# Kernel optimization log

Measured on AMD Instinct MI355X. Metric: run time of the kernel, lower is better.

Reference implementation:

```python
import jax, jax.numpy as jnp
import numpy as np

DIM = 256
NUM_HEADS = 4
HEAD_DIM = DIM // NUM_HEADS
SCALE = HEAD_DIM ** -0.5
LOGIT_CLAMP = 6.0


def _conv1x1(x, w, b):
    # x: (B,C,H,W), w: (Cout,Cin), b: (Cout,)
    return jnp.einsum('bchw,oc->bohw', x, w) + b[None, :, None, None]


def setup_inputs() -> dict:
    key = jax.random.key(0)
    ks = jax.random.split(key, 10)
    B, C, H, W = 8, DIM, 48, 48
    init = lambda k, shape, fan_in: jax.random.normal(k, shape, jnp.float32) * (fan_in ** -0.5)
    return {
        'src_feat': jax.random.normal(ks[0], (B, C, H, W), jnp.float32),
        'tgt_feat': jax.random.normal(ks[1], (B, C, H, W), jnp.float32),
        'qw': init(ks[2], (DIM, DIM), DIM), 'qb': jnp.zeros((DIM,), jnp.float32),
        'kw': init(ks[3], (DIM, DIM), DIM), 'kb': jnp.zeros((DIM,), jnp.float32),
        'vw': init(ks[4], (DIM, DIM), DIM), 'vb': jnp.zeros((DIM,), jnp.float32),
        'ow': init(ks[5], (DIM, DIM), DIM), 'ob': jnp.zeros((DIM,), jnp.float32),
    }


def reference(src_feat, tgt_feat, qw, qb, kw, kb, vw, vb, ow, ob):
    B, C, H, W = src_feat.shape
    N = H * W
    Q = _conv1x1(src_feat, qw, qb)
    K = _conv1x1(tgt_feat, kw, kb)
    V = _conv1x1(tgt_feat, vw, vb)
    # (B,C,H,W) -> (B,heads,head_dim,N) -> (B,heads,N,head_dim)
    to_heads = lambda t: t.reshape(B, NUM_HEADS, HEAD_DIM, N).transpose(0, 1, 3, 2)
    Qh, Kh, Vh = to_heads(Q), to_heads(K), to_heads(V)
    attn = jnp.einsum('bhnd,bhmd->bhnm', Qh, Kh) * SCALE
    attn = jnp.clip(attn, -LOGIT_CLAMP, LOGIT_CLAMP)
    attn = jax.nn.softmax(attn, axis=-1)
    out = jnp.einsum('bhnm,bhmd->bhnd', attn, Vh)
    out = out.transpose(0, 1, 3, 2).reshape(B, C, H, W)
    return _conv1x1(out, ow, ob)
```

## Files before the change

kernel.cpp:

```cpp
#include <hip/hip_runtime.h>
#include <hip/hip_bf16.h>

#define DIM 256
#define NHEADS 4
#define HDIM 64
#define NPIX 2304
#define NBATCH 8
#define KCN 72
#define NTN 144
#define SCALE_L2E 0.18033688011112042f
#define CLAMP_L2E 8.656170245332781f

typedef __hip_bfloat16 bf16;
typedef __bf16 bf16x8 __attribute__((ext_vector_type(8)));
typedef float  f32x4  __attribute__((ext_vector_type(4)));
typedef float  f32x16 __attribute__((ext_vector_type(16)));

__device__ __forceinline__ unsigned int pack2bf(float a, float b) {
    __hip_bfloat162 h = __float22bfloat162_rn(float2{a, b});
    union { __hip_bfloat162 h; unsigned int u; } c; c.h = h;
    return c.u;
}

__global__ __launch_bounds__(256) void cvt_w_kernel(
    const float* __restrict__ w0, const float* __restrict__ w1,
    const float* __restrict__ w2, const float* __restrict__ w3,
    bf16* __restrict__ out)
{
    const int sel = blockIdx.y;
    const float* src = sel == 0 ? w0 : sel == 1 ? w1 : sel == 2 ? w2 : w3;
    const int i = blockIdx.x * 256 + threadIdx.x;
    const int m = i >> 5, c0 = (i & 31) * 8;
    const int mh = m >> 7, mt = (m >> 4) & 7, lo = m & 15;
    const int kc = c0 >> 5, hi = (c0 >> 3) & 3;
    float4 a = *(const float4*)(src + i * 8);
    float4 b = *(const float4*)(src + i * 8 + 4);
    uint4 u;
    u.x = pack2bf(a.x, a.y); u.y = pack2bf(a.z, a.w);
    u.z = pack2bf(b.x, b.y); u.w = pack2bf(b.z, b.w);
    const size_t fb = (((size_t)(mh * 8 + kc)) * 8 + mt) * 512 + (hi * 16 + lo) * 8;
    *(uint4*)(void*)(out + (size_t)sel * 65536 + fb) = u;
}

__global__ __launch_bounds__(256) void txp_kernel(
    const float* __restrict__ src, const float* __restrict__ tgt,
    bf16* __restrict__ oS, bf16* __restrict__ oT)
{
    const int b = blockIdx.z & 7;
    const float* in = (blockIdx.z >> 3) ? tgt : src;
    bf16* out = (blockIdx.z >> 3) ? oT : oS;
    const int n0 = blockIdx.x * 64, c0 = blockIdx.y * 64;
    __shared__ float tile[64][65];
    const int t = threadIdx.x;
#pragma unroll
    for (int i = 0; i < 4; ++i) {
        int idx = t + i * 256;
        int cl = idx >> 4, n4 = (idx & 15) * 4;
        float4 v = *(const float4*)(in + ((size_t)b * DIM + c0 + cl) * NPIX + n0 + n4);
        tile[cl][n4] = v.x; tile[cl][n4 + 1] = v.y;
        tile[cl][n4 + 2] = v.z; tile[cl][n4 + 3] = v.w;
    }
    __syncthreads();
#pragma unroll
    for (int i = 0; i < 2; ++i) {
        int idx = t + i * 256;
        int nl = idx >> 3, c8 = (idx & 7) * 8;
        uint4 u;
        u.x = pack2bf(tile[c8 + 0][nl], tile[c8 + 1][nl]);
        u.y = pack2bf(tile[c8 + 2][nl], tile[c8 + 3][nl]);
        u.z = pack2bf(tile[c8 + 4][nl], tile[c8 + 5][nl]);
        u.w = pack2bf(tile[c8 + 6][nl], tile[c8 + 7][nl]);
        const int n = n0 + nl, c = c0 + c8;
        const size_t fb = (((size_t)(b * NTN + (n >> 4))) * 8 + (c >> 5)) * 512
                        + ((((c >> 3) & 3) * 16) + (n & 15)) * 8;
        *(uint4*)(void*)(out + fb) = u;
    }
}

__device__ __forceinline__ void conv_core(
    const bf16* __restrict__ xp, const bf16* __restrict__ wp,
    int wk, f32x4 (&acc)[8])
{
#pragma unroll
    for (int mt = 0; mt < 8; ++mt) acc[mt] = (f32x4){0.f, 0.f, 0.f, 0.f};

    const int kbase = wk * 4;
    bf16x8 a = *(const bf16x8*)(const void*)(xp + (size_t)kbase * 512);
    bf16x8 bfr[8];
#pragma unroll
    for (int mt = 0; mt < 8; ++mt)
        bfr[mt] = *(const bf16x8*)(const void*)(wp + (size_t)(kbase * 8 + mt) * 512);

#pragma unroll
    for (int ki = 0; ki < 4; ++ki) {
        const int kn = kbase + ((ki + 1) & 3);
        bf16x8 a2 = *(const bf16x8*)(const void*)(xp + (size_t)kn * 512);
        bf16x8 bfr2[8];
#pragma unroll
        for (int mt = 0; mt < 8; ++mt)
            bfr2[mt] = *(const bf16x8*)(const void*)(wp + (size_t)(kn * 8 + mt) * 512);
#pragma unroll
        for (int mt = 0; mt < 8; ++mt)
            acc[mt] = __builtin_amdgcn_mfma_f32_16x16x32_bf16(a, bfr[mt], acc[mt], 0, 0, 0);
        a = a2;
#pragma unroll
        for (int mt = 0; mt < 8; ++mt) bfr[mt] = bfr2[mt];
    }
}

__global__ __launch_bounds__(256, 3) void conv_qkv_kernel(
    const bf16* __restrict__ XS, const bf16* __restrict__ XT,
    const bf16* __restrict__ Wbf,
    const float* __restrict__ qb, const float* __restrict__ kb2,
    const float* __restrict__ vb2,
    bf16* __restrict__ Qt, bf16* __restrict__ Kt, bf16* __restrict__ Vt)
{
    const int b  = blockIdx.z;
    const int sel = blockIdx.y >> 1, mh = blockIdx.y & 1;
    const int n0 = blockIdx.x * 32;
    const int w  = threadIdx.x >> 6, l = threadIdx.x & 63;
    const int wn = w & 1, wk = w >> 1;
    const int lo = l & 15, hi = l >> 4;

    __shared__ float red[2][64][36];

    const bf16* X = sel == 0 ? XS : XT;
    const float* bias = sel == 0 ? qb : sel == 1 ? kb2 : vb2;
    const float scale = sel == 0 ? SCALE_L2E : 1.0f;
    bf16* Yb = sel == 0 ? Qt : sel == 1 ? Kt : Vt;

    const int ntile = blockIdx.x * 2 + wn;
    const bf16* xp = X + ((size_t)(b * NTN + ntile) * 8) * 512 + l * 8;
    const bf16* wp = Wbf + (size_t)sel * 65536 + (size_t)mh * 32768 + l * 8;

    f32x4 acc[8];
    conv_core(xp, wp, wk, acc);

    if (wk == 1) {
#pragma unroll
        for (int mt = 0; mt < 8; ++mt)
            *(float4*)&red[wn][l][mt * 4] = make_float4(acc[mt][0], acc[mt][1],
                                                        acc[mt][2], acc[mt][3]);
    }
    __syncthreads();
    if (wk != 0) return;

#pragma unroll
    for (int mt = 0; mt < 8; ++mt) {
        float4 v = *(float4*)&red[wn][l][mt * 4];
        acc[mt][0] += v.x; acc[mt][1] += v.y; acc[mt][2] += v.z; acc[mt][3] += v.w;
    }

    const int nb = n0 + wn * 16 + hi * 4;
#pragma unroll
    for (int mt = 0; mt < 8; ++mt) {
        const int m = mh * 128 + mt * 16 + lo;
        const float bv = bias[m];
        if (sel < 2) {
            const int h = m >> 6, d = m & 63;
            const size_t fb = (((size_t)(b * NHEADS + h) * KCN + (nb >> 5)) * 4 + (d >> 4)) * 512
                            + ((((d >> 3) & 1) * 32) + (nb & 31)) * 8 + (d & 7);
#pragma unroll
            for (int r = 0; r < 4; ++r)
                Yb[fb + r * 8] = __float2bfloat16((acc[mt][r] + bv) * scale);
        } else {
            const int h = m >> 6, dv = m & 63;
            const size_t fb = ((((size_t)(b * NHEADS + h) * KCN + (nb >> 5)) * 2 + ((nb >> 4) & 1)) * 2
                               + (dv >> 5)) * 512
                            + ((((nb >> 3) & 1) * 32) + (dv & 31)) * 8 + (nb & 7);
            uint2 u = make_uint2(pack2bf(acc[mt][0] + bv, acc[mt][1] + bv),
                                 pack2bf(acc[mt][2] + bv, acc[mt][3] + bv));
            *(uint2*)(void*)(Yb + fb) = u;
        }
    }
}

__global__ __launch_bounds__(256, 3) void conv_out_kernel(
    const bf16* __restrict__ X, const bf16* __restrict__ Wb,
    const float* __restrict__ bias, float* __restrict__ Yf)
{
    const int b  = blockIdx.z, mh = blockIdx.y;
    const int n0 = blockIdx.x * 32;
    const int w  = threadIdx.x >> 6, l = threadIdx.x & 63;
    const int wn = w & 1, wk = w >> 1;
    const int lo = l & 15, hi = l >> 4;

    __shared__ float red[2][64][36];

    const int ntile = blockIdx.x * 2 + wn;
    const bf16* xp = X + ((size_t)(b * NTN + ntile) * 8) * 512 + l * 8;
    const bf16* wp = Wb + (size_t)mh * 32768 + l * 8;

    f32x4 acc[8];
    conv_core(xp, wp, wk, acc);

    if (wk == 1) {
#pragma unroll
        for (int mt = 0; mt < 8; ++mt)
            *(float4*)&red[wn][l][mt * 4] = make_float4(acc[mt][0], acc[mt][1],
                                                        acc[mt][2], acc[mt][3]);
    }
    __syncthreads();
    if (wk != 0) return;

#pragma unroll
    for (int mt = 0; mt < 8; ++mt) {
        float4 v = *(float4*)&red[wn][l][mt * 4];
        acc[mt][0] += v.x; acc[mt][1] += v.y; acc[mt][2] += v.z; acc[mt][3] += v.w;
    }

    const int nb = n0 + wn * 16 + hi * 4;
#pragma unroll
    for (int mt = 0; mt < 8; ++mt) {
        const int m = mh * 128 + mt * 16 + lo;
        const float bv = bias[m];
        float4 v = make_float4(acc[mt][0] + bv, acc[mt][1] + bv,
                               acc[mt][2] + bv, acc[mt][3] + bv);
        *(float4*)(void*)(Yf + ((size_t)b * DIM + m) * NPIX + nb) = v;
    }
}

__global__ __launch_bounds__(256, 2) void attn_kernel(
    const bf16* __restrict__ Qt, const bf16* __restrict__ Kt,
    const bf16* __restrict__ Vt, bf16* __restrict__ Op)
{
    const int b = blockIdx.z, h = blockIdx.y;
    const int w = threadIdx.x >> 6;
    const int wq = w & 1, wk = w >> 1;
    const int l = threadIdx.x & 63;
    const int ln = l & 31, h2 = l >> 5;
    const int bh = b * NHEADS + h;
    const int qt = blockIdx.x;

    __shared__ float red[2][2][32][68];
    __shared__ float lred[2][2][32];

    const bf16* QB = Qt + ((size_t)bh * KCN + qt * 4 + wq * 2) * 2048 + l * 8;
    const bf16* KB = Kt + (size_t)bh * KCN * 2048 + l * 8;
    const bf16* VB = Vt + (size_t)bh * KCN * 2048 + l * 8;

    bf16x8 qf[2][4];
#pragma unroll
    for (int qs = 0; qs < 2; ++qs)
#pragma unroll
        for (int dk = 0; dk < 4; ++dk)
            qf[qs][dk] = *(const bf16x8*)(const void*)(QB + qs * 2048 + dk * 512);

    f32x16 oacc[2][2];
#pragma unroll
    for (int qs = 0; qs < 2; ++qs)
#pragma unroll
        for (int dt = 0; dt < 2; ++dt)
#pragma unroll
            for (int r = 0; r < 16; ++r) oacc[qs][dt][r] = 0.f;
    float lsum[2] = {0.f, 0.f};

    bf16x8 kfA[4], kfB[4];
    bf16x8 vfA[2][2], vfB[2][2];

    auto load_chunk = [&](int kc_, bf16x8 (&kfD)[4], bf16x8 (&vfD)[2][2]) {
        const bf16* KBn = KB + (size_t)kc_ * 2048;
        const bf16* VBn = VB + (size_t)kc_ * 2048;
#pragma unroll
        for (int dk = 0; dk < 4; ++dk)
            kfD[dk] = *(const bf16x8*)(const void*)(KBn + dk * 512);
#pragma unroll
        for (int kb = 0; kb < 2; ++kb)
#pragma unroll
            for (int dt = 0; dt < 2; ++dt)
                vfD[kb][dt] = *(const bf16x8*)(const void*)(VBn + kb * 1024 + dt * 512);
    };

    auto compute = [&](const bf16x8 (&kfX)[4], const bf16x8 (&vfX)[2][2]) {
#pragma unroll
        for (int qs = 0; qs < 2; ++qs) {
            f32x16 s;
#pragma unroll
            for (int r = 0; r < 16; ++r) s[r] = 0.f;
#pragma unroll
            for (int dk = 0; dk < 4; ++dk)
                s = __builtin_amdgcn_mfma_f32_32x32x16_bf16(kfX[dk], qf[qs][dk], s, 0, 0, 0);

            float ls = 0.f;
            unsigned int pk[8];
#pragma unroll
            for (int p = 0; p < 8; ++p) {
                float ea = __builtin_amdgcn_exp2f(
                    __builtin_amdgcn_fmed3f(s[2 * p],     -CLAMP_L2E, CLAMP_L2E));
                float eb = __builtin_amdgcn_exp2f(
                    __builtin_amdgcn_fmed3f(s[2 * p + 1], -CLAMP_L2E, CLAMP_L2E));
                ls += ea + eb;
                pk[p] = pack2bf(ea, eb);
            }
            lsum[qs] += ls;

            unsigned int c00 = pk[0], c02 = pk[2], c01 = pk[1], c03 = pk[3];
            unsigned int c10 = pk[4], c12 = pk[6], c11 = pk[5], c13 = pk[7];
            asm("v_permlane32_swap_b32 %0, %1" : "+v"(c00), "+v"(c02));
            asm("v_permlane32_swap_b32 %0, %1" : "+v"(c01), "+v"(c03));
            asm("v_permlane32_swap_b32 %0, %1" : "+v"(c10), "+v"(c12));
            asm("v_permlane32_swap_b32 %0, %1" : "+v"(c11), "+v"(c13));
            union { unsigned int u[4]; bf16x8 v; } pb0, pb1;
            pb0.u[0] = c00; pb0.u[1] = c01; pb0.u[2] = c02; pb0.u[3] = c03;
            pb1.u[0] = c10; pb1.u[1] = c11; pb1.u[2] = c12; pb1.u[3] = c13;

#pragma unroll
            for (int dt = 0; dt < 2; ++dt) {
                oacc[qs][dt] = __builtin_amdgcn_mfma_f32_32x32x16_bf16(vfX[0][dt], pb0.v, oacc[qs][dt], 0, 0, 0);
                oacc[qs][dt] = __builtin_amdgcn_mfma_f32_32x32x16_bf16(vfX[1][dt], pb1.v, oacc[qs][dt], 0, 0, 0);
            }
        }
    };

    load_chunk(wk, kfA, vfA);
    for (int i = 0; i < 36; i += 2) {
        load_chunk(wk + 2 * (i + 1), kfB, vfB);
        compute(kfA, vfA);
        load_chunk(i + 2 < 36 ? wk + 2 * (i + 2) : wk, kfA, vfA);
        compute(kfB, vfB);
    }

#pragma unroll
    for (int qs = 0; qs < 2; ++qs) lsum[qs] += __shfl_xor(lsum[qs], 32);
    if (wk == 1) {
        if (h2 == 0) { lred[wq][0][ln] = lsum[0]; lred[wq][1][ln] = lsum[1]; }
#pragma unroll
        for (int qs = 0; qs < 2; ++qs)
#pragma unroll
            for (int dt = 0; dt < 2; ++dt)
#pragma unroll
                for (int g = 0; g < 4; ++g) {
                    float4 v = make_float4(oacc[qs][dt][g * 4 + 0], oacc[qs][dt][g * 4 + 1],
                                           oacc[qs][dt][g * 4 + 2], oacc[qs][dt][g * 4 + 3]);
                    *(float4*)&red[wq][qs][ln][dt * 32 + g * 8 + h2 * 4] = v;
                }
    }
    __syncthreads();

    if (wk == 0) {
#pragma unroll
        for (int qs = 0; qs < 2; ++qs) {
#pragma unroll
            for (int dt = 0; dt < 2; ++dt)
#pragma unroll
                for (int g = 0; g < 4; ++g) {
                    float4 v = *(float4*)&red[wq][qs][ln][dt * 32 + g * 8 + h2 * 4];
                    oacc[qs][dt][g * 4 + 0] += v.x; oacc[qs][dt][g * 4 + 1] += v.y;
                    oacc[qs][dt][g * 4 + 2] += v.z; oacc[qs][dt][g * 4 + 3] += v.w;
                }
            const float inv = 1.f / (lsum[qs] + lred[wq][qs][ln]);

            const int ntile = qt * 8 + wq * 4 + qs * 2 + (ln >> 4);
            bf16* opb = Op + (((size_t)(b * NTN + ntile)) * 8 + h * 2) * 512
                      + (ln & 15) * 8 + h2 * 4;
#pragma unroll
            for (int dt = 0; dt < 2; ++dt)
#pragma unroll
                for (int g = 0; g < 4; ++g) {
                    float v0 = oacc[qs][dt][g * 4 + 0] * inv;
                    float v1 = oacc[qs][dt][g * 4 + 1] * inv;
                    float v2 = oacc[qs][dt][g * 4 + 2] * inv;
                    float v3 = oacc[qs][dt][g * 4 + 3] * inv;
                    uint2 u = make_uint2(pack2bf(v0, v1), pack2bf(v2, v3));
                    *(uint2*)(void*)(opb + (size_t)dt * 512 + g * 128) = u;
                }
        }
    }
}

extern "C" void kernel_launch(void* const* d_in, const int* in_sizes, int n_in,
                              void* d_out, int out_size, void* d_ws, size_t ws_size,
                              hipStream_t stream) {
    const float* src = (const float*)d_in[0];
    const float* tgt = (const float*)d_in[1];
    const float* qw  = (const float*)d_in[2];
    const float* qb  = (const float*)d_in[3];
    const float* kw  = (const float*)d_in[4];
    const float* kb  = (const float*)d_in[5];
    const float* vw  = (const float*)d_in[6];
    const float* vb  = (const float*)d_in[7];
    const float* ow  = (const float*)d_in[8];
    const float* ob  = (const float*)d_in[9];
    float* out = (float*)d_out;

    const size_t TEN = (size_t)NBATCH * DIM * NPIX;
    bf16* Wbf  = (bf16*)d_ws;
    bf16* XbfS = Wbf  + 4 * 65536;
    bf16* XbfT = XbfS + TEN;
    bf16* Qt   = XbfT + TEN;
    bf16* Kt   = Qt   + TEN;
    bf16* Vt   = Kt   + TEN;
    bf16* Op   = Vt   + TEN;

    cvt_w_kernel<<<dim3(32, 4, 1), 256, 0, stream>>>(qw, kw, vw, ow, Wbf);
    txp_kernel<<<dim3(NPIX / 64, DIM / 64, 2 * NBATCH), 256, 0, stream>>>(src, tgt, XbfS, XbfT);

    conv_qkv_kernel<<<dim3(NPIX / 32, 6, NBATCH), 256, 0, stream>>>(
        XbfS, XbfT, Wbf, qb, kb, vb, Qt, Kt, Vt);

    attn_kernel<<<dim3(NPIX / 128, NHEADS, NBATCH), 256, 0, stream>>>(Qt, Kt, Vt, Op);

    conv_out_kernel<<<dim3(NPIX / 32, 2, NBATCH), 256, 0, stream>>>(
        Op, Wbf + 3 * 65536, ob, out);
}
```

Baseline: 120.5 us.

## Fuse input transpose and bf16 conversion into QKV projection kernel

Removes the separate transpose kernel and the bf16 staging buffers for src and tgt. Each QKV conv block now loads its fp32 input slice directly, transposes it through shared memory and packs it into bf16 MFMA fragment layout in LDS before the GEMM. This drops one launch and an intermediate write and read, but the fp32 inputs are re-read by multiple blocks (per projection and half) and LDS usage grows, which may reduce occupancy.

```diff
diff --git a/kernel.cpp b/kernel.cpp
--- a/kernel.cpp
+++ b/kernel.cpp
@@ -42,112 +42,104 @@
     *(uint4*)(void*)(out + (size_t)sel * 65536 + fb) = u;
 }
 
-__global__ __launch_bounds__(256) void txp_kernel(
-    const float* __restrict__ src, const float* __restrict__ tgt,
-    bf16* __restrict__ oS, bf16* __restrict__ oT)
-{
-    const int b = blockIdx.z & 7;
-    const float* in = (blockIdx.z >> 3) ? tgt : src;
-    bf16* out = (blockIdx.z >> 3) ? oT : oS;
-    const int n0 = blockIdx.x * 64, c0 = blockIdx.y * 64;
-    __shared__ float tile[64][65];
-    const int t = threadIdx.x;
-#pragma unroll
-    for (int i = 0; i < 4; ++i) {
-        int idx = t + i * 256;
-        int cl = idx >> 4, n4 = (idx & 15) * 4;
-        float4 v = *(const float4*)(in + ((size_t)b * DIM + c0 + cl) * NPIX + n0 + n4);
-        tile[cl][n4] = v.x; tile[cl][n4 + 1] = v.y;
-        tile[cl][n4 + 2] = v.z; tile[cl][n4 + 3] = v.w;
-    }
-    __syncthreads();
-#pragma unroll
-    for (int i = 0; i < 2; ++i) {
-        int idx = t + i * 256;
-        int nl = idx >> 3, c8 = (idx & 7) * 8;
-        uint4 u;
-        u.x = pack2bf(tile[c8 + 0][nl], tile[c8 + 1][nl]);
-        u.y = pack2bf(tile[c8 + 2][nl], tile[c8 + 3][nl]);
-        u.z = pack2bf(tile[c8 + 4][nl], tile[c8 + 5][nl]);
-        u.w = pack2bf(tile[c8 + 6][nl], tile[c8 + 7][nl]);
-        const int n = n0 + nl, c = c0 + c8;
-        const size_t fb = (((size_t)(b * NTN + (n >> 4))) * 8 + (c >> 5)) * 512
-                        + ((((c >> 3) & 3) * 16) + (n & 15)) * 8;
-        *(uint4*)(void*)(out + fb) = u;
-    }
-}
-
-__device__ __forceinline__ void conv_core(
-    const bf16* __restrict__ xp, const bf16* __restrict__ wp,
-    int wk, f32x4 (&acc)[8])
-{
-#pragma unroll
-    for (int mt = 0; mt < 8; ++mt) acc[mt] = (f32x4){0.f, 0.f, 0.f, 0.f};
-
-    const int kbase = wk * 4;
-    bf16x8 a = *(const bf16x8*)(const void*)(xp + (size_t)kbase * 512);
-    bf16x8 bfr[8];
-#pragma unroll
-    for (int mt = 0; mt < 8; ++mt)
-        bfr[mt] = *(const bf16x8*)(const void*)(wp + (size_t)(kbase * 8 + mt) * 512);
-
-#pragma unroll
-    for (int ki = 0; ki < 4; ++ki) {
-        const int kn = kbase + ((ki + 1) & 3);
-        bf16x8 a2 = *(const bf16x8*)(const void*)(xp + (size_t)kn * 512);
-        bf16x8 bfr2[8];
-#pragma unroll
-        for (int mt = 0; mt < 8; ++mt)
-            bfr2[mt] = *(const bf16x8*)(const void*)(wp + (size_t)(kn * 8 + mt) * 512);
-#pragma unroll
-        for (int mt = 0; mt < 8; ++mt)
-            acc[mt] = __builtin_amdgcn_mfma_f32_16x16x32_bf16(a, bfr[mt], acc[mt], 0, 0, 0);
-        a = a2;
-#pragma unroll
-        for (int mt = 0; mt < 8; ++mt) bfr[mt] = bfr2[mt];
-    }
-}
-
 __global__ __launch_bounds__(256, 3) void conv_qkv_kernel(
-    const bf16* __restrict__ XS, const bf16* __restrict__ XT,
+    const float* __restrict__ srcf, const float* __restrict__ tgtf,
     const bf16* __restrict__ Wbf,
     const float* __restrict__ qb, const float* __restrict__ kb2,
     const float* __restrict__ vb2,
     bf16* __restrict__ Qt, bf16* __restrict__ Kt, bf16* __restrict__ Vt)
 {
+    __shared__ __align__(16) unsigned char smem[50176];
+    float (*tile)[33] = reinterpret_cast<float(*)[33]>(smem);
+    bf16* fx = reinterpret_cast<bf16*>(smem + 33792);
+    float (*red)[36] = reinterpret_cast<float(*)[36]>(smem);
+
     const int b  = blockIdx.z;
     const int sel = blockIdx.y >> 1, mh = blockIdx.y & 1;
     const int n0 = blockIdx.x * 32;
-    const int w  = threadIdx.x >> 6, l = threadIdx.x & 63;
+    const int t  = threadIdx.x;
+    const int w  = t >> 6, l = t & 63;
     const int wn = w & 1, wk = w >> 1;
     const int lo = l & 15, hi = l >> 4;
 
-    __shared__ float red[2][64][36];
-
-    const bf16* X = sel == 0 ? XS : XT;
+    const float* Xf = sel == 0 ? srcf : tgtf;
     const float* bias = sel == 0 ? qb : sel == 1 ? kb2 : vb2;
     const float scale = sel == 0 ? SCALE_L2E : 1.0f;
     bf16* Yb = sel == 0 ? Qt : sel == 1 ? Kt : Vt;
 
-    const int ntile = blockIdx.x * 2 + wn;
-    const bf16* xp = X + ((size_t)(b * NTN + ntile) * 8) * 512 + l * 8;
-    const bf16* wp = Wbf + (size_t)sel * 65536 + (size_t)mh * 32768 + l * 8;
+    {
+        const int trow = t >> 3, tf = t & 7;
+#pragma unroll
+        for (int p = 0; p < 8; ++p) {
+            const int c = trow + p * 32;
+            float4 v = *(const float4*)(Xf + ((size_t)b * DIM + c) * NPIX + n0 + tf * 4);
+            tile[c][tf * 4 + 0] = v.x; tile[c][tf * 4 + 1] = v.y;
+            tile[c][tf * 4 + 2] = v.z; tile[c][tf * 4 + 3] = v.w;
+        }
+    }
+    __syncthreads();
+
+    {
+        const int pwn = t >> 7, r = t & 127;
+        const int pkc = r >> 4, phi = (r >> 2) & 3, plo0 = (r & 3) * 4;
+#pragma unroll
+        for (int lo2 = 0; lo2 < 4; ++lo2) {
+            const int plo = plo0 + lo2;
+            const int row = pkc * 32 + phi * 8;
+            const int col = pwn * 16 + plo;
+            uint4 u;
+            u.x = pack2bf(tile[row + 0][col], tile[row + 1][col]);
+            u.y = pack2bf(tile[row + 2][col], tile[row + 3][col]);
+            u.z = pack2bf(tile[row + 4][col], tile[row + 5][col]);
+            u.w = pack2bf(tile[row + 6][col], tile[row + 7][col]);
+            *(uint4*)(void*)&fx[(size_t)pwn * 4096 + pkc * 512 + (phi * 16 + plo) * 8] = u;
+        }
+    }
+    __syncthreads();
+
+    const bf16* fxw = fx + (size_t)wn * 4096;
+    const bf16* wp  = Wbf + (size_t)sel * 65536 + (size_t)mh * 32768 + l * 8;
 
     f32x4 acc[8];
-    conv_core(xp, wp, wk, acc);
-
+#pragma unroll
+    for (int mt = 0; mt < 8; ++mt) acc[mt] = (f32x4){0.f, 0.f, 0.f, 0.f};
+
+    const int kbase = wk * 4;
+    bf16x8 a = *(const bf16x8*)(const void*)(fxw + kbase * 512 + l * 8);
+    bf16x8 bfr[8];
+#pragma unroll
+    for (int mt = 0; mt < 8; ++mt)
+        bfr[mt] = *(const bf16x8*)(const void*)(wp + (size_t)(kbase * 8 + mt) * 512);
+
+#pragma unroll
+    for (int ki = 0; ki < 4; ++ki) {
+        const int kn = kbase + ((ki + 1) & 3);
+        bf16x8 a2 = *(const bf16x8*)(const void*)(fxw + kn * 512 + l * 8);
+        bf16x8 bfr2[8];
+#pragma unroll
+        for (int mt = 0; mt < 8; ++mt)
+            bfr2[mt] = *(const bf16x8*)(const void*)(wp + (size_t)(kn * 8 + mt) * 512);
+#pragma unroll
+        for (int mt = 0; mt < 8; ++mt)
+            acc[mt] = __builtin_amdgcn_mfma_f32_16x16x32_bf16(a, bfr[mt], acc[mt], 0, 0, 0);
+        a = a2;
+#pragma unroll
+        for (int mt = 0; mt < 8; ++mt) bfr[mt] = bfr2[mt];
+    }
+
+    __syncthreads();
     if (wk == 1) {
 #pragma unroll
         for (int mt = 0; mt < 8; ++mt)
-            *(float4*)&red[wn][l][mt * 4] = make_float4(acc[mt][0], acc[mt][1],
-                                                        acc[mt][2], acc[mt][3]);
+            *(float4*)&red[wn * 64 + l][mt * 4] = make_float4(acc[mt][0], acc[mt][1],
+                                                              acc[mt][2], acc[mt][3]);
     }
     __syncthreads();
     if (wk != 0) return;
 
 #pragma unroll
     for (int mt = 0; mt < 8; ++mt) {
-        float4 v = *(float4*)&red[wn][l][mt * 4];
+        float4 v = *(float4*)&red[wn * 64 + l][mt * 4];
         acc[mt][0] += v.x; acc[mt][1] += v.y; acc[mt][2] += v.z; acc[mt][3] += v.w;
     }
 
@@ -192,7 +184,31 @@
     const bf16* wp = Wb + (size_t)mh * 32768 + l * 8;
 
     f32x4 acc[8];
-    conv_core(xp, wp, wk, acc);
+#pragma unroll
+    for (int mt = 0; mt < 8; ++mt) acc[mt] = (f32x4){0.f, 0.f, 0.f, 0.f};
+
+    const int kbase = wk * 4;
+    bf16x8 a = *(const bf16x8*)(const void*)(xp + (size_t)kbase * 512);
+    bf16x8 bfr[8];
+#pragma unroll
+    for (int mt = 0; mt < 8; ++mt)
+        bfr[mt] = *(const bf16x8*)(const void*)(wp + (size_t)(kbase * 8 + mt) * 512);
+
+#pragma unroll
+    for (int ki = 0; ki < 4; ++ki) {
+        const int kn = kbase + ((ki + 1) & 3);
+        bf16x8 a2 = *(const bf16x8*)(const void*)(xp + (size_t)kn * 512);
+        bf16x8 bfr2[8];
+#pragma unroll
+        for (int mt = 0; mt < 8; ++mt)
+            bfr2[mt] = *(const bf16x8*)(const void*)(wp + (size_t)(kn * 8 + mt) * 512);
+#pragma unroll
+        for (int mt = 0; mt < 8; ++mt)
+            acc[mt] = __builtin_amdgcn_mfma_f32_16x16x32_bf16(a, bfr[mt], acc[mt], 0, 0, 0);
+        a = a2;
+#pragma unroll
+        for (int mt = 0; mt < 8; ++mt) bfr[mt] = bfr2[mt];
+    }
 
     if (wk == 1) {
 #pragma unroll
@@ -385,18 +401,15 @@
 
     const size_t TEN = (size_t)NBATCH * DIM * NPIX;
     bf16* Wbf  = (bf16*)d_ws;
-    bf16* XbfS = Wbf  + 4 * 65536;
-    bf16* XbfT = XbfS + TEN;
-    bf16* Qt   = XbfT + TEN;
-    bf16* Kt   = Qt   + TEN;
-    bf16* Vt   = Kt   + TEN;
-    bf16* Op   = Vt   + TEN;
+    bf16* Qt   = Wbf + 4 * 65536;
+    bf16* Kt   = Qt  + TEN;
+    bf16* Vt   = Kt  + TEN;
+    bf16* Op   = Vt  + TEN;
 
     cvt_w_kernel<<<dim3(32, 4, 1), 256, 0, stream>>>(qw, kw, vw, ow, Wbf);
-    txp_kernel<<<dim3(NPIX / 64, DIM / 64, 2 * NBATCH), 256, 0, stream>>>(src, tgt, XbfS, XbfT);
 
     conv_qkv_kernel<<<dim3(NPIX / 32, 6, NBATCH), 256, 0, stream>>>(
-        XbfS, XbfT, Wbf, qb, kb, vb, Qt, Kt, Vt);
+        src, tgt, Wbf, qb, kb, vb, Qt, Kt, Vt);
 
     attn_kernel<<<dim3(NPIX / 128, NHEADS, NBATCH), 256, 0, stream>>>(Qt, Kt, Vt, Op);
 
```

Measured after the change: 119.5 us. Within noise of the previous version (-0.8%).
